# Kernel tuning notes

Measured on AMD Instinct MI355X. Metric: run time of the kernel, lower is better.

The kernel has to match this reference:

```python
import jax, jax.numpy as jnp
import numpy as np

EMBED_SIZE = 1024
HEADS = 16
HEAD_DIM = EMBED_SIZE // HEADS


def setup_inputs() -> dict:
    key = jax.random.key(0)
    ks = jax.random.split(key, 8)
    B, S = 4, 2048
    inp = {
        "values": jax.random.normal(ks[0], (B, S, EMBED_SIZE), dtype=jnp.float32),
        "keys": jax.random.normal(ks[1], (B, S, EMBED_SIZE), dtype=jnp.float32),
        "query": jax.random.normal(ks[2], (B, S, EMBED_SIZE), dtype=jnp.float32),
        "mask": jnp.zeros((B, S), dtype=jnp.int32),  # accepted but unused, as in the original
        # per-head projection weights (nn.Linear(head_dim, head_dim, bias=False)): y = x @ W.T
        "Wv": jax.random.normal(ks[3], (HEAD_DIM, HEAD_DIM), dtype=jnp.float32) / np.sqrt(HEAD_DIM),
        "Wk": jax.random.normal(ks[4], (HEAD_DIM, HEAD_DIM), dtype=jnp.float32) / np.sqrt(HEAD_DIM),
        "Wq": jax.random.normal(ks[5], (HEAD_DIM, HEAD_DIM), dtype=jnp.float32) / np.sqrt(HEAD_DIM),
        # fc_out: nn.Linear(embed_size, embed_size)
        "Wo": jax.random.normal(ks[6], (EMBED_SIZE, EMBED_SIZE), dtype=jnp.float32) / np.sqrt(EMBED_SIZE),
        "bo": jax.random.normal(ks[7], (EMBED_SIZE,), dtype=jnp.float32) * 0.01,
    }
    return inp


def reference(values, keys, query, mask, Wv, Wk, Wq, Wo, bo):
    N, S, _ = query.shape
    # reshape to (N, len, heads, head_dim)
    v = values.reshape(N, S, HEADS, HEAD_DIM)
    k = keys.reshape(N, S, HEADS, HEAD_DIM)
    q = query.reshape(N, S, HEADS, HEAD_DIM)
    # per-head linear projections (shared across heads), y = x @ W.T
    v = jnp.einsum('nlhd,ed->nlhe', v, Wv)
    k = jnp.einsum('nlhd,ed->nlhe', k, Wk)
    q = jnp.einsum('nlhd,ed->nlhe', q, Wq)
    # attention scores: (N, H, Q, K), scaled by sqrt(embed_size) as in the original
    energy = jnp.einsum('nqhd,nkhd->nhqk', q, k)
    attention = jax.nn.softmax(energy / jnp.sqrt(jnp.float32(EMBED_SIZE)), axis=3)
    out = jnp.einsum('nhql,nlhd->nqhd', attention, v).reshape(N, S, EMBED_SIZE)
    out = out @ Wo.T + bo
    return out
```

## Files before the change

### kernel.cpp

```cpp
#include <hip/hip_runtime.h>


typedef __attribute__((ext_vector_type(8))) short short8;
typedef __attribute__((ext_vector_type(4))) float f32x4;
typedef __attribute__((ext_vector_type(2))) unsigned int uint2v;

constexpr int Bn = 4, Sn = 2048, Hn = 16, Dn = 64, En = 1024;
constexpr int HEADELEMS = Bn * Hn * Sn * Dn;

__device__ __forceinline__ unsigned short f2bf(float f) {
  union { float f; unsigned u; } x; x.f = f;
  unsigned u = x.u;
  return (unsigned short)((u + 0x7FFFu + ((u >> 16) & 1u)) >> 16);
}

__device__ __forceinline__ short8 pack8(f32x4 a, f32x4 b) {
  short8 r;
  r[0] = (short)f2bf(a[0]); r[1] = (short)f2bf(a[1]);
  r[2] = (short)f2bf(a[2]); r[3] = (short)f2bf(a[3]);
  r[4] = (short)f2bf(b[0]); r[5] = (short)f2bf(b[1]);
  r[6] = (short)f2bf(b[2]); r[7] = (short)f2bf(b[3]);
  return r;
}

__device__ __forceinline__ float fexp2(float x) {
#if __has_builtin(__builtin_amdgcn_exp2f)
  return __builtin_amdgcn_exp2f(x);
#else
  return exp2f(x);
#endif
}

__device__ __forceinline__ unsigned cvtpk_bf16(float lo, float hi) {
  unsigned r;
  asm("v_cvt_pk_bf16_f32 %0, %1, %2" : "=v"(r) : "v"(lo), "v"(hi));
  return r;
}

__device__ __forceinline__ void gload_lds16(const unsigned short* g, unsigned short* l) {
  __builtin_amdgcn_global_load_lds((const __attribute__((address_space(1))) void*)g,
                                   (__attribute__((address_space(3))) void*)l, 16, 0, 0);
}

__global__ __launch_bounds__(256) void wqk_kernel(const float* __restrict__ Wq,
                                                  const float* __restrict__ Wk,
                                                  unsigned short* __restrict__ Mt) {
  __shared__ float lq[4096], lk[4096];
  const int t = threadIdx.x;
  for (int i = t; i < 4096; i += 256) { lq[i] = Wq[i]; lk[i] = Wk[i]; }
  __syncthreads();
  const float scale = 0.04508422f;
#pragma unroll
  for (int i = 0; i < 16; ++i) {
    int o = i * 256 + t;
    int c = o >> 6, d = o & 63;
    float acc = 0.f;
    for (int e = 0; e < 64; ++e) acc += lq[e * 64 + d] * lk[e * 64 + c];
    Mt[c * 64 + d] = f2bf(acc * scale);
  }
}

__global__ __launch_bounds__(256) void wvo_kernel(const float* __restrict__ Wv,
                                                  const float* __restrict__ Wo,
                                                  unsigned short* __restrict__ Ut) {
  __shared__ float lv[4096];
  const int e = blockIdx.x, t = threadIdx.x;
  for (int i = t; i < 4096; i += 256) lv[i] = Wv[i];
  __syncthreads();
#pragma unroll
  for (int i = 0; i < 4; ++i) {
    int hd = i * 256 + t;
    int h = hd >> 6, d = hd & 63;
    float acc = 0.f;
    const float* wrow = Wo + e * 1024 + h * 64;
    for (int dp = 0; dp < 64; ++dp) acc += lv[dp * 64 + d] * wrow[dp];
    Ut[e * 1024 + hd] = f2bf(acc);
  }
}

__global__ __launch_bounds__(256) void prep_kernel(
    const float* __restrict__ vin, const float* __restrict__ kin,
    const float* __restrict__ qin, const unsigned short* __restrict__ Mt,
    unsigned short* __restrict__ qp, unsigned short* __restrict__ kbuf,
    unsigned short* __restrict__ vT) {
  __shared__ alignas(16) unsigned short ldsQ[64][72];
  __shared__ alignas(16) unsigned short ldsV[64][72];

  const int blk = blockIdx.x;
  const int st = blk & 31, h = (blk >> 5) & 15, b = blk >> 9;
  const int s0 = st * 64;
  const int t = threadIdx.x;
  const int wid = t >> 6, lane = t & 63, lg = lane >> 4, li = lane & 15;

  const int row = t >> 2, seg = t & 3;
  const int srcoff = (b * Sn + s0 + row) * En + h * 64 + seg * 16;

  {
    const f32x4* ks = reinterpret_cast<const f32x4*>(kin + srcoff);
    unsigned short* dst = kbuf + ((b * Hn + h) * Sn + s0 + row) * Dn + seg * 16;
    *reinterpret_cast<short8*>(dst) = pack8(ks[0], ks[1]);
    *reinterpret_cast<short8*>(dst + 8) = pack8(ks[2], ks[3]);
  }
  {
    const f32x4* vs = reinterpret_cast<const f32x4*>(vin + srcoff);
    *reinterpret_cast<short8*>(&ldsV[row][seg * 16]) = pack8(vs[0], vs[1]);
    *reinterpret_cast<short8*>(&ldsV[row][seg * 16 + 8]) = pack8(vs[2], vs[3]);
    const f32x4* qs = reinterpret_cast<const f32x4*>(qin + srcoff);
    *reinterpret_cast<short8*>(&ldsQ[row][seg * 16]) = pack8(qs[0], qs[1]);
    *reinterpret_cast<short8*>(&ldsQ[row][seg * 16 + 8]) = pack8(qs[2], qs[3]);
  }
  __syncthreads();

  {
    const int d = t >> 2, ss = t & 3;
    short8 o0, o1;
#pragma unroll
    for (int j = 0; j < 8; ++j) o0[j] = (short)ldsV[ss * 16 + j][d];
#pragma unroll
    for (int j = 0; j < 8; ++j) o1[j] = (short)ldsV[ss * 16 + 8 + j][d];
    unsigned short* dst = vT + ((b * Hn + h) * Dn + d) * Sn + s0 + ss * 16;
    *reinterpret_cast<short8*>(dst) = o0;
    *reinterpret_cast<short8*>(dst + 8) = o1;
  }

  {
    short8 qa0 = *reinterpret_cast<const short8*>(&ldsQ[wid * 16 + li][lg * 8]);
    short8 qa1 = *reinterpret_cast<const short8*>(&ldsQ[wid * 16 + li][32 + lg * 8]);
    f32x4 acc[4] = {{0,0,0,0},{0,0,0,0},{0,0,0,0},{0,0,0,0}};
#pragma unroll
    for (int cb = 0; cb < 4; ++cb) {
      short8 b0 = *reinterpret_cast<const short8*>(Mt + (cb * 16 + li) * 64 + lg * 8);
      short8 b1 = *reinterpret_cast<const short8*>(Mt + (cb * 16 + li) * 64 + 32 + lg * 8);
      acc[cb] = __builtin_amdgcn_mfma_f32_16x16x32_bf16(qa0, b0, acc[cb], 0, 0, 0);
      acc[cb] = __builtin_amdgcn_mfma_f32_16x16x32_bf16(qa1, b1, acc[cb], 0, 0, 0);
    }
    unsigned short* dst = qp + ((b * Hn + h) * Sn + s0 + wid * 16 + lg * 4) * Dn;
#pragma unroll
    for (int cb = 0; cb < 4; ++cb)
#pragma unroll
      for (int r = 0; r < 4; ++r) dst[r * Dn + cb * 16 + li] = f2bf(acc[cb][r]);
  }
}

__global__ __launch_bounds__(256) void attn_kernel(
    const unsigned short* __restrict__ qp, const unsigned short* __restrict__ kbuf,
    const unsigned short* __restrict__ vT, unsigned short* __restrict__ pv) {
  __shared__ alignas(16) unsigned short ldsK[2][4096];
  __shared__ alignas(16) unsigned short ldsV[2][4096];
  __shared__ alignas(16) unsigned short ldsP[4][32][72];

  const int bid = blockIdx.x;
  const int xcd = bid & 7, j = bid >> 3;
  const int bh = ((j & 7) << 3) + xcd;
  const int qt = j >> 3;
  const int b = bh >> 4, h = bh & 15;

  const int t = threadIdx.x;
  const int wid = t >> 6, lane = t & 63, lg = lane >> 4, li = lane & 15;
  const int bhS = bh * Sn;
  const int q0 = qt * 128 + wid * 32;

  const int koff0 = ((lg ^ (li & 7)) << 3);

  const int srow = lane >> 3, sgrp = (lane & 7) ^ srow;
  const unsigned short* ksrc = kbuf + (size_t)(bhS + wid * 32 + srow) * Dn + sgrp * 8;
  const unsigned short* vsrc = vT + ((size_t)bh * Dn + (wid - 2) * 32 + srow) * Sn + sgrp * 8;

  short8 qb[2][2];
#pragma unroll
  for (int rb = 0; rb < 2; ++rb)
#pragma unroll
    for (int kc = 0; kc < 2; ++kc)
      qb[rb][kc] = *reinterpret_cast<const short8*>(
          qp + (size_t)(bhS + q0 + rb * 16 + li) * Dn + kc * 32 + lg * 8);

  f32x4 o[2][4];
#pragma unroll
  for (int rb = 0; rb < 2; ++rb)
#pragma unroll
    for (int i = 0; i < 4; ++i) o[rb][i] = f32x4{0, 0, 0, 0};
  float l0 = 0.f, l1 = 0.f;

  auto stage = [&](int buf, int kt) {
    if (wid < 2) {
      const unsigned short* src = ksrc + (size_t)kt * 4096;
      unsigned short* dst = &ldsK[buf][wid * 2048];
#pragma unroll
      for (int jj = 0; jj < 4; ++jj) gload_lds16(src + jj * 512, dst + jj * 512);
    } else {
      const unsigned short* src = vsrc + kt * 64;
      unsigned short* dst = &ldsV[buf][(wid - 2) * 2048];
#pragma unroll
      for (int jj = 0; jj < 4; ++jj) gload_lds16(src + jj * 16384, dst + jj * 512);
    }
  };

  stage(0, 0);
  __syncthreads();
  int cur = 0;

  for (int kt = 0; kt < 32; ++kt) {
    if (kt < 31) stage(cur ^ 1, kt + 1);

    const unsigned short* Kb = ldsK[cur];
#pragma unroll
    for (int cb = 0; cb < 4; ++cb) {
      const int ra = (cb * 16 + li) * 64 + koff0;
      short8 ka0 = *reinterpret_cast<const short8*>(&Kb[ra]);
      short8 ka1 = *reinterpret_cast<const short8*>(&Kb[ra ^ 32]);
      f32x4 s0 = {0, 0, 0, 0}, s1 = {0, 0, 0, 0};
      s0 = __builtin_amdgcn_mfma_f32_16x16x32_bf16(ka0, qb[0][0], s0, 0, 0, 0);
      s0 = __builtin_amdgcn_mfma_f32_16x16x32_bf16(ka1, qb[0][1], s0, 0, 0, 0);
      s1 = __builtin_amdgcn_mfma_f32_16x16x32_bf16(ka0, qb[1][0], s1, 0, 0, 0);
      s1 = __builtin_amdgcn_mfma_f32_16x16x32_bf16(ka1, qb[1][1], s1, 0, 0, 0);
      float p0[4], p1[4];
#pragma unroll
      for (int r = 0; r < 4; ++r) {
        p0[r] = fexp2(s0[r]); l0 += p0[r];
        p1[r] = fexp2(s1[r]); l1 += p1[r];
      }
      uint2v w0, w1;
      w0[0] = cvtpk_bf16(p0[0], p0[1]); w0[1] = cvtpk_bf16(p0[2], p0[3]);
      w1[0] = cvtpk_bf16(p1[0], p1[1]); w1[1] = cvtpk_bf16(p1[2], p1[3]);
      *reinterpret_cast<uint2v*>(&ldsP[wid][li][cb * 16 + 4 * lg]) = w0;
      *reinterpret_cast<uint2v*>(&ldsP[wid][16 + li][cb * 16 + 4 * lg]) = w1;
    }

    short8 pa[2][2];
#pragma unroll
    for (int rb = 0; rb < 2; ++rb)
#pragma unroll
      for (int kc = 0; kc < 2; ++kc)
        pa[rb][kc] = *reinterpret_cast<const short8*>(
            &ldsP[wid][rb * 16 + li][kc * 32 + lg * 8]);

    const unsigned short* Vb = ldsV[cur];
#pragma unroll
    for (int db = 0; db < 4; ++db) {
      const int va = (db * 16 + li) * 64 + koff0;
      short8 vb0 = *reinterpret_cast<const short8*>(&Vb[va]);
      short8 vb1 = *reinterpret_cast<const short8*>(&Vb[va ^ 32]);
      o[0][db] = __builtin_amdgcn_mfma_f32_16x16x32_bf16(pa[0][0], vb0, o[0][db], 0, 0, 0);
      o[0][db] = __builtin_amdgcn_mfma_f32_16x16x32_bf16(pa[0][1], vb1, o[0][db], 0, 0, 0);
      o[1][db] = __builtin_amdgcn_mfma_f32_16x16x32_bf16(pa[1][0], vb0, o[1][db], 0, 0, 0);
      o[1][db] = __builtin_amdgcn_mfma_f32_16x16x32_bf16(pa[1][1], vb1, o[1][db], 0, 0, 0);
    }

    __syncthreads();
    cur ^= 1;
  }

  l0 += __shfl_xor(l0, 16, 64); l0 += __shfl_xor(l0, 32, 64);
  l1 += __shfl_xor(l1, 16, 64); l1 += __shfl_xor(l1, 32, 64);
#pragma unroll
  for (int r = 0; r < 4; ++r) {
    float i0 = 1.f / __shfl(l0, 4 * lg + r, 16);
    float i1 = 1.f / __shfl(l1, 4 * lg + r, 16);
    const int sg = q0 + 4 * lg + r;
    unsigned short* d0 = pv + ((size_t)(b * Sn + sg) * Hn + h) * Dn + li;
    unsigned short* d1 = d0 + (size_t)16 * Hn * Dn;
#pragma unroll
    for (int db = 0; db < 4; ++db) {
      d0[db * 16] = f2bf(o[0][db][r] * i0);
      d1[db * 16] = f2bf(o[1][db][r] * i1);
    }
  }
}

__global__ __launch_bounds__(256) void ogemm_kernel(
    const unsigned short* __restrict__ pvm, const unsigned short* __restrict__ Ut,
    const float* __restrict__ bo, float* __restrict__ out) {
  __shared__ alignas(16) unsigned short ldsA[128][72];
  __shared__ alignas(16) unsigned short ldsB[128][72];

  const int en = blockIdx.x, mt = blockIdx.y;
  const int t = threadIdx.x;
  const int wid = t >> 6, lane = t & 63, lg = lane >> 4, li = lane & 15;
  const int wr = wid >> 1, wc = wid & 1;
  const int m0 = mt * 128, e0 = en * 128;

  f32x4 acc[4][4];
#pragma unroll
  for (int i = 0; i < 4; ++i)
#pragma unroll
    for (int j = 0; j < 4; ++j) acc[i][j] = f32x4{0, 0, 0, 0};

  const int row = t >> 1, half = t & 1;
  for (int kt = 0; kt < 16; ++kt) {
    const int k0 = kt * 64;
    {
      const short8* as = reinterpret_cast<const short8*>(pvm + (m0 + row) * 1024 + k0 + half * 32);
      const short8* bs = reinterpret_cast<const short8*>(Ut + (e0 + row) * 1024 + k0 + half * 32);
#pragma unroll
      for (int i = 0; i < 4; ++i) {
        *reinterpret_cast<short8*>(&ldsA[row][half * 32 + i * 8]) = as[i];
        *reinterpret_cast<short8*>(&ldsB[row][half * 32 + i * 8]) = bs[i];
      }
    }
    __syncthreads();
#pragma unroll
    for (int kc = 0; kc < 2; ++kc) {
      short8 af[4], bf[4];
#pragma unroll
      for (int mr = 0; mr < 4; ++mr)
        af[mr] = *reinterpret_cast<const short8*>(&ldsA[wr * 64 + mr * 16 + li][kc * 32 + lg * 8]);
#pragma unroll
      for (int nr = 0; nr < 4; ++nr)
        bf[nr] = *reinterpret_cast<const short8*>(&ldsB[wc * 64 + nr * 16 + li][kc * 32 + lg * 8]);
#pragma unroll
      for (int mr = 0; mr < 4; ++mr)
#pragma unroll
        for (int nr = 0; nr < 4; ++nr)
          acc[mr][nr] = __builtin_amdgcn_mfma_f32_16x16x32_bf16(af[mr], bf[nr], acc[mr][nr], 0, 0, 0);
    }
    __syncthreads();
  }

#pragma unroll
  for (int nr = 0; nr < 4; ++nr) {
    int col = e0 + wc * 64 + nr * 16 + li;
    float bias = bo[col];
#pragma unroll
    for (int mr = 0; mr < 4; ++mr)
#pragma unroll
      for (int r = 0; r < 4; ++r)
        out[(m0 + wr * 64 + mr * 16 + lg * 4 + r) * 1024 + col] = acc[mr][nr][r] + bias;
  }
}

extern "C" void kernel_launch(void* const* d_in, const int* in_sizes, int n_in,
                              void* d_out, int out_size, void* d_ws, size_t ws_size,
                              hipStream_t stream) {
  const float* vin = (const float*)d_in[0];
  const float* kin = (const float*)d_in[1];
  const float* qin = (const float*)d_in[2];
  const float* Wv = (const float*)d_in[4];
  const float* Wk = (const float*)d_in[5];
  const float* Wq = (const float*)d_in[6];
  const float* Wo = (const float*)d_in[7];
  const float* bo = (const float*)d_in[8];
  float* out = (float*)d_out;

  unsigned short* qp = (unsigned short*)d_ws;
  unsigned short* kb = qp + HEADELEMS;
  unsigned short* vT = kb + HEADELEMS;
  unsigned short* pv = vT + HEADELEMS;
  unsigned short* Ut = pv + HEADELEMS;
  unsigned short* Mt = Ut + En * En;

  wqk_kernel<<<1, 256, 0, stream>>>(Wq, Wk, Mt);
  wvo_kernel<<<1024, 256, 0, stream>>>(Wv, Wo, Ut);
  prep_kernel<<<2048, 256, 0, stream>>>(vin, kin, qin, Mt, qp, kb, vT);
  attn_kernel<<<1024, 256, 0, stream>>>(qp, kb, vT, pv);
  ogemm_kernel<<<dim3(8, 64), 256, 0, stream>>>(pv, Ut, bo, out);
}
```

Before: 322.3 us.

## Fold QK weight product onto keys, fuse weight kernels, widen attention blocks, pipeline output GEMM

```diff
diff --git a/kernel.cpp b/kernel.cpp
--- a/kernel.cpp
+++ b/kernel.cpp
@@ -42,27 +42,10 @@
                                    (__attribute__((address_space(3))) void*)l, 16, 0, 0);
 }
 
-__global__ __launch_bounds__(256) void wqk_kernel(const float* __restrict__ Wq,
-                                                  const float* __restrict__ Wk,
-                                                  unsigned short* __restrict__ Mt) {
-  __shared__ float lq[4096], lk[4096];
-  const int t = threadIdx.x;
-  for (int i = t; i < 4096; i += 256) { lq[i] = Wq[i]; lk[i] = Wk[i]; }
-  __syncthreads();
-  const float scale = 0.04508422f;
-#pragma unroll
-  for (int i = 0; i < 16; ++i) {
-    int o = i * 256 + t;
-    int c = o >> 6, d = o & 63;
-    float acc = 0.f;
-    for (int e = 0; e < 64; ++e) acc += lq[e * 64 + d] * lk[e * 64 + c];
-    Mt[c * 64 + d] = f2bf(acc * scale);
-  }
-}
-
-__global__ __launch_bounds__(256) void wvo_kernel(const float* __restrict__ Wv,
-                                                  const float* __restrict__ Wo,
-                                                  unsigned short* __restrict__ Ut) {
+__global__ __launch_bounds__(256) void wfused_kernel(
+    const float* __restrict__ Wq, const float* __restrict__ Wk,
+    const float* __restrict__ Wv, const float* __restrict__ Wo,
+    unsigned short* __restrict__ Ut, unsigned short* __restrict__ Mg) {
   __shared__ float lv[4096];
   const int e = blockIdx.x, t = threadIdx.x;
   for (int i = t; i < 4096; i += 256) lv[i] = Wv[i];
@@ -76,14 +59,20 @@
     for (int dp = 0; dp < 64; ++dp) acc += lv[dp * 64 + d] * wrow[dp];
     Ut[e * 1024 + hd] = f2bf(acc);
   }
+  if (e < 16) {
+    int idx = e * 256 + t;
+    int d = idx >> 6, c = idx & 63;
+    float acc = 0.f;
+    for (int o = 0; o < 64; ++o) acc += Wq[o * 64 + d] * Wk[o * 64 + c];
+    Mg[idx] = f2bf(acc * 0.04508422f);
+  }
 }
 
 __global__ __launch_bounds__(256) void prep_kernel(
     const float* __restrict__ vin, const float* __restrict__ kin,
-    const float* __restrict__ qin, const unsigned short* __restrict__ Mt,
-    unsigned short* __restrict__ qp, unsigned short* __restrict__ kbuf,
-    unsigned short* __restrict__ vT) {
-  __shared__ alignas(16) unsigned short ldsQ[64][72];
+    const unsigned short* __restrict__ Mg,
+    unsigned short* __restrict__ kp, unsigned short* __restrict__ vT) {
+  __shared__ alignas(16) unsigned short ldsK[64][72];
   __shared__ alignas(16) unsigned short ldsV[64][72];
 
   const int blk = blockIdx.x;
@@ -91,63 +80,64 @@
   const int s0 = st * 64;
   const int t = threadIdx.x;
   const int wid = t >> 6, lane = t & 63, lg = lane >> 4, li = lane & 15;
-
   const int row = t >> 2, seg = t & 3;
   const int srcoff = (b * Sn + s0 + row) * En + h * 64 + seg * 16;
 
   {
     const f32x4* ks = reinterpret_cast<const f32x4*>(kin + srcoff);
-    unsigned short* dst = kbuf + ((b * Hn + h) * Sn + s0 + row) * Dn + seg * 16;
-    *reinterpret_cast<short8*>(dst) = pack8(ks[0], ks[1]);
-    *reinterpret_cast<short8*>(dst + 8) = pack8(ks[2], ks[3]);
-  }
-  {
+    *reinterpret_cast<short8*>(&ldsK[row][seg * 16]) = pack8(ks[0], ks[1]);
+    *reinterpret_cast<short8*>(&ldsK[row][seg * 16 + 8]) = pack8(ks[2], ks[3]);
     const f32x4* vs = reinterpret_cast<const f32x4*>(vin + srcoff);
     *reinterpret_cast<short8*>(&ldsV[row][seg * 16]) = pack8(vs[0], vs[1]);
     *reinterpret_cast<short8*>(&ldsV[row][seg * 16 + 8]) = pack8(vs[2], vs[3]);
-    const f32x4* qs = reinterpret_cast<const f32x4*>(qin + srcoff);
-    *reinterpret_cast<short8*>(&ldsQ[row][seg * 16]) = pack8(qs[0], qs[1]);
-    *reinterpret_cast<short8*>(&ldsQ[row][seg * 16 + 8]) = pack8(qs[2], qs[3]);
   }
   __syncthreads();
 
   {
-    const int d = t >> 2, ss = t & 3;
+    const int d = lane, sq = wid;
+    unsigned short col[16];
+#pragma unroll
+    for (int j = 0; j < 16; ++j) col[j] = ldsV[sq * 16 + j][d];
     short8 o0, o1;
 #pragma unroll
-    for (int j = 0; j < 8; ++j) o0[j] = (short)ldsV[ss * 16 + j][d];
-#pragma unroll
-    for (int j = 0; j < 8; ++j) o1[j] = (short)ldsV[ss * 16 + 8 + j][d];
-    unsigned short* dst = vT + ((b * Hn + h) * Dn + d) * Sn + s0 + ss * 16;
+    for (int j = 0; j < 8; ++j) { o0[j] = (short)col[j]; o1[j] = (short)col[8 + j]; }
+    unsigned short* dst = vT + ((size_t)((b * Hn + h) * Dn + d)) * Sn + s0 + sq * 16;
     *reinterpret_cast<short8*>(dst) = o0;
     *reinterpret_cast<short8*>(dst + 8) = o1;
   }
 
   {
-    short8 qa0 = *reinterpret_cast<const short8*>(&ldsQ[wid * 16 + li][lg * 8]);
-    short8 qa1 = *reinterpret_cast<const short8*>(&ldsQ[wid * 16 + li][32 + lg * 8]);
+    short8 ka0 = *reinterpret_cast<const short8*>(&ldsK[wid * 16 + li][lg * 8]);
+    short8 ka1 = *reinterpret_cast<const short8*>(&ldsK[wid * 16 + li][32 + lg * 8]);
     f32x4 acc[4] = {{0,0,0,0},{0,0,0,0},{0,0,0,0},{0,0,0,0}};
 #pragma unroll
     for (int cb = 0; cb < 4; ++cb) {
-      short8 b0 = *reinterpret_cast<const short8*>(Mt + (cb * 16 + li) * 64 + lg * 8);
-      short8 b1 = *reinterpret_cast<const short8*>(Mt + (cb * 16 + li) * 64 + 32 + lg * 8);
-      acc[cb] = __builtin_amdgcn_mfma_f32_16x16x32_bf16(qa0, b0, acc[cb], 0, 0, 0);
-      acc[cb] = __builtin_amdgcn_mfma_f32_16x16x32_bf16(qa1, b1, acc[cb], 0, 0, 0);
-    }
-    unsigned short* dst = qp + ((b * Hn + h) * Sn + s0 + wid * 16 + lg * 4) * Dn;
+      short8 b0 = *reinterpret_cast<const short8*>(Mg + (cb * 16 + li) * 64 + lg * 8);
+      short8 b1 = *reinterpret_cast<const short8*>(Mg + (cb * 16 + li) * 64 + 32 + lg * 8);
+      acc[cb] = __builtin_amdgcn_mfma_f32_16x16x32_bf16(ka0, b0, acc[cb], 0, 0, 0);
+      acc[cb] = __builtin_amdgcn_mfma_f32_16x16x32_bf16(ka1, b1, acc[cb], 0, 0, 0);
+    }
 #pragma unroll
     for (int cb = 0; cb < 4; ++cb)
 #pragma unroll
-      for (int r = 0; r < 4; ++r) dst[r * Dn + cb * 16 + li] = f2bf(acc[cb][r]);
-  }
-}
-
-__global__ __launch_bounds__(256) void attn_kernel(
-    const unsigned short* __restrict__ qp, const unsigned short* __restrict__ kbuf,
+      for (int r = 0; r < 4; ++r)
+        ldsK[wid * 16 + lg * 4 + r][cb * 16 + li] = f2bf(acc[cb][r]);
+  }
+  __syncthreads();
+
+  {
+    unsigned short* dst = kp + ((size_t)((b * Hn + h) * Sn + s0 + row)) * Dn + seg * 16;
+    *reinterpret_cast<short8*>(dst) = *reinterpret_cast<const short8*>(&ldsK[row][seg * 16]);
+    *reinterpret_cast<short8*>(dst + 8) = *reinterpret_cast<const short8*>(&ldsK[row][seg * 16 + 8]);
+  }
+}
+
+__global__ __launch_bounds__(512, 4) void attn_kernel(
+    const float* __restrict__ qin, const unsigned short* __restrict__ kp,
     const unsigned short* __restrict__ vT, unsigned short* __restrict__ pv) {
   __shared__ alignas(16) unsigned short ldsK[2][4096];
   __shared__ alignas(16) unsigned short ldsV[2][4096];
-  __shared__ alignas(16) unsigned short ldsP[4][32][72];
+  __shared__ alignas(16) unsigned short ldsP[8][32][72];
 
   const int bid = blockIdx.x;
   const int xcd = bid & 7, j = bid >> 3;
@@ -158,21 +148,24 @@
   const int t = threadIdx.x;
   const int wid = t >> 6, lane = t & 63, lg = lane >> 4, li = lane & 15;
   const int bhS = bh * Sn;
-  const int q0 = qt * 128 + wid * 32;
+  const int q0 = qt * 256 + wid * 32;
 
   const int koff0 = ((lg ^ (li & 7)) << 3);
 
-  const int srow = lane >> 3, sgrp = (lane & 7) ^ srow;
-  const unsigned short* ksrc = kbuf + (size_t)(bhS + wid * 32 + srow) * Dn + sgrp * 8;
-  const unsigned short* vsrc = vT + ((size_t)bh * Dn + (wid - 2) * 32 + srow) * Sn + sgrp * 8;
+  const int sr = t >> 3, sg = t & 7;
+  const unsigned short* ksrc = kp + (size_t)(bhS + sr) * Dn + ((sg ^ (sr & 7)) << 3);
+  const unsigned short* vsrc = vT + ((size_t)bh * Dn + sr) * Sn + ((sg ^ (sr & 7)) << 3);
 
   short8 qb[2][2];
 #pragma unroll
   for (int rb = 0; rb < 2; ++rb)
 #pragma unroll
-    for (int kc = 0; kc < 2; ++kc)
-      qb[rb][kc] = *reinterpret_cast<const short8*>(
-          qp + (size_t)(bhS + q0 + rb * 16 + li) * Dn + kc * 32 + lg * 8);
+    for (int kc = 0; kc < 2; ++kc) {
+      const float* qrow = qin + (size_t)(b * Sn + q0 + rb * 16 + li) * En + h * 64 + kc * 32 + lg * 8;
+      f32x4 a = *reinterpret_cast<const f32x4*>(qrow);
+      f32x4 c = *reinterpret_cast<const f32x4*>(qrow + 4);
+      qb[rb][kc] = pack8(a, c);
+    }
 
   f32x4 o[2][4];
 #pragma unroll
@@ -182,17 +175,8 @@
   float l0 = 0.f, l1 = 0.f;
 
   auto stage = [&](int buf, int kt) {
-    if (wid < 2) {
-      const unsigned short* src = ksrc + (size_t)kt * 4096;
-      unsigned short* dst = &ldsK[buf][wid * 2048];
-#pragma unroll
-      for (int jj = 0; jj < 4; ++jj) gload_lds16(src + jj * 512, dst + jj * 512);
-    } else {
-      const unsigned short* src = vsrc + kt * 64;
-      unsigned short* dst = &ldsV[buf][(wid - 2) * 2048];
-#pragma unroll
-      for (int jj = 0; jj < 4; ++jj) gload_lds16(src + jj * 16384, dst + jj * 512);
-    }
+    gload_lds16(ksrc + (size_t)kt * 4096, &ldsK[buf][t * 8]);
+    gload_lds16(vsrc + kt * 64, &ldsV[buf][t * 8]);
   };
 
   stage(0, 0);
@@ -256,8 +240,8 @@
   for (int r = 0; r < 4; ++r) {
     float i0 = 1.f / __shfl(l0, 4 * lg + r, 16);
     float i1 = 1.f / __shfl(l1, 4 * lg + r, 16);
-    const int sg = q0 + 4 * lg + r;
-    unsigned short* d0 = pv + ((size_t)(b * Sn + sg) * Hn + h) * Dn + li;
+    const int sg2 = q0 + 4 * lg + r;
+    unsigned short* d0 = pv + ((size_t)(b * Sn + sg2) * Hn + h) * Dn + li;
     unsigned short* d1 = d0 + (size_t)16 * Hn * Dn;
 #pragma unroll
     for (int db = 0; db < 4; ++db) {
@@ -270,10 +254,12 @@
 __global__ __launch_bounds__(256) void ogemm_kernel(
     const unsigned short* __restrict__ pvm, const unsigned short* __restrict__ Ut,
     const float* __restrict__ bo, float* __restrict__ out) {
-  __shared__ alignas(16) unsigned short ldsA[128][72];
-  __shared__ alignas(16) unsigned short ldsB[128][72];
-
-  const int en = blockIdx.x, mt = blockIdx.y;
+  __shared__ alignas(16) unsigned short ldsA[2][8192];
+  __shared__ alignas(16) unsigned short ldsB[2][8192];
+
+  const int bid = blockIdx.x;
+  const int wg = (bid & 7) * 64 + (bid >> 3);
+  const int en = wg & 7, mt = wg >> 3;
   const int t = threadIdx.x;
   const int wid = t >> 6, lane = t & 63, lg = lane >> 4, li = lane & 15;
   const int wr = wid >> 1, wc = wid & 1;
@@ -283,48 +269,60 @@
 #pragma unroll
   for (int i = 0; i < 4; ++i)
 #pragma unroll
-    for (int j = 0; j < 4; ++j) acc[i][j] = f32x4{0, 0, 0, 0};
-
-  const int row = t >> 1, half = t & 1;
+    for (int jj = 0; jj < 4; ++jj) acc[i][jj] = f32x4{0, 0, 0, 0};
+
+  const int r0 = t >> 3, G = t & 7;
+
+  auto stage = [&](int buf, int k0) {
+#pragma unroll
+    for (int rd = 0; rd < 4; ++rd) {
+      const int r = r0 + rd * 32;
+      const int so = ((G ^ (r & 7)) << 3);
+      gload_lds16(pvm + (size_t)(m0 + r) * 1024 + k0 + so, &ldsA[buf][rd * 2048 + t * 8]);
+      gload_lds16(Ut + (size_t)(e0 + r) * 1024 + k0 + so, &ldsB[buf][rd * 2048 + t * 8]);
+    }
+  };
+
+  stage(0, 0);
+  __syncthreads();
+  int cur = 0;
+
   for (int kt = 0; kt < 16; ++kt) {
-    const int k0 = kt * 64;
-    {
-      const short8* as = reinterpret_cast<const short8*>(pvm + (m0 + row) * 1024 + k0 + half * 32);
-      const short8* bs = reinterpret_cast<const short8*>(Ut + (e0 + row) * 1024 + k0 + half * 32);
-#pragma unroll
-      for (int i = 0; i < 4; ++i) {
-        *reinterpret_cast<short8*>(&ldsA[row][half * 32 + i * 8]) = as[i];
-        *reinterpret_cast<short8*>(&ldsB[row][half * 32 + i * 8]) = bs[i];
+    if (kt < 15) stage(cur ^ 1, (kt + 1) * 64);
+#pragma unroll
+    for (int kc = 0; kc < 2; ++kc) {
+      short8 af[4], bfr[4];
+#pragma unroll
+      for (int mr = 0; mr < 4; ++mr) {
+        const int row = wr * 64 + mr * 16 + li;
+        af[mr] = *reinterpret_cast<const short8*>(
+            &ldsA[cur][row * 64 + (((kc * 4 + lg) ^ (li & 7)) << 3)]);
       }
+#pragma unroll
+      for (int nr = 0; nr < 4; ++nr) {
+        const int row = wc * 64 + nr * 16 + li;
+        bfr[nr] = *reinterpret_cast<const short8*>(
+            &ldsB[cur][row * 64 + (((kc * 4 + lg) ^ (li & 7)) << 3)]);
+      }
+#pragma unroll
+      for (int mr = 0; mr < 4; ++mr)
+#pragma unroll
+        for (int nr = 0; nr < 4; ++nr)
+          acc[mr][nr] = __builtin_amdgcn_mfma_f32_16x16x32_bf16(af[mr], bfr[nr], acc[mr][nr], 0, 0, 0);
     }
     __syncthreads();
-#pragma unroll
-    for (int kc = 0; kc < 2; ++kc) {
-      short8 af[4], bf[4];
-#pragma unroll
-      for (int mr = 0; mr < 4; ++mr)
-        af[mr] = *reinterpret_cast<const short8*>(&ldsA[wr * 64 + mr * 16 + li][kc * 32 + lg * 8]);
-#pragma unroll
-      for (int nr = 0; nr < 4; ++nr)
-        bf[nr] = *reinterpret_cast<const short8*>(&ldsB[wc * 64 + nr * 16 + li][kc * 32 + lg * 8]);
-#pragma unroll
-      for (int mr = 0; mr < 4; ++mr)
-#pragma unroll
-        for (int nr = 0; nr < 4; ++nr)
-          acc[mr][nr] = __builtin_amdgcn_mfma_f32_16x16x32_bf16(af[mr], bf[nr], acc[mr][nr], 0, 0, 0);
-    }
-    __syncthreads();
+    cur ^= 1;
   }
 
 #pragma unroll
   for (int nr = 0; nr < 4; ++nr) {
-    int col = e0 + wc * 64 + nr * 16 + li;
-    float bias = bo[col];
+    const int col = e0 + wc * 64 + nr * 16 + li;
+    const float bias = bo[col];
 #pragma unroll
     for (int mr = 0; mr < 4; ++mr)
 #pragma unroll
       for (int r = 0; r < 4; ++r)
-        out[(m0 + wr * 64 + mr * 16 + lg * 4 + r) * 1024 + col] = acc[mr][nr][r] + bias;
+        out[(size_t)(m0 + wr * 64 + mr * 16 + lg * 4 + r) * 1024 + col] = acc[mr][nr][r] + bias;
   }
 }
 
@@ -341,16 +339,14 @@
   const float* bo = (const float*)d_in[8];
   float* out = (float*)d_out;
 
-  unsigned short* qp = (unsigned short*)d_ws;
-  unsigned short* kb = qp + HEADELEMS;
-  unsigned short* vT = kb + HEADELEMS;
+  unsigned short* kp = (unsigned short*)d_ws;
+  unsigned short* vT = kp + HEADELEMS;
   unsigned short* pv = vT + HEADELEMS;
   unsigned short* Ut = pv + HEADELEMS;
-  unsigned short* Mt = Ut + En * En;
-
-  wqk_kernel<<<1, 256, 0, stream>>>(Wq, Wk, Mt);
-  wvo_kernel<<<1024, 256, 0, stream>>>(Wv, Wo, Ut);
-  prep_kernel<<<2048, 256, 0, stream>>>(vin, kin, qin, Mt, qp, kb, vT);
-  attn_kernel<<<1024, 256, 0, stream>>>(qp, kb, vT, pv);
-  ogemm_kernel<<<dim3(8, 64), 256, 0, stream>>>(pv, Ut, bo, out);
-}
+  unsigned short* Mg = Ut + En * En;
+
+  wfused_kernel<<<1024, 256, 0, stream>>>(Wq, Wk, Wv, Wo, Ut, Mg);
+  prep_kernel<<<2048, 256, 0, stream>>>(vin, kin, Mg, kp, vT);
+  attn_kernel<<<512, 512, 0, stream>>>(qin, kp, vT, pv);
+  ogemm_kernel<<<512, 256, 0, stream>>>(pv, Ut, bo, out);
+}
```

New measurement: 274.2 us. 14.9% less time.
